# Kernel optimization log

Measured on AMD Instinct MI355X. Metric: run time of the kernel, lower is better.

The kernel has to match this reference:

```python
import jax, jax.numpy as jnp
import numpy as np

B, T, P, I, H, O = 64, 32, 64, 256, 128, 88  # batch, time_steps, pitch_steps, input, hidden, output


def setup_inputs() -> dict:
    key = jax.random.key(0)
    ks = jax.random.split(key, 11)
    s = 0.05
    return {
        "x": jax.random.normal(ks[0], (B, T, P, I), jnp.float32),
        # stacked [fwd, bwd] direction weights, PyTorch LSTM gate order (i, f, g, o)
        "Wt_ih": jax.random.normal(ks[1], (2, 4 * H, I), jnp.float32) * s,
        "Wt_hh": jax.random.normal(ks[2], (2, 4 * H, H), jnp.float32) * s,
        "bt_ih": jax.random.normal(ks[3], (2, 4 * H), jnp.float32) * s,
        "bt_hh": jax.random.normal(ks[4], (2, 4 * H), jnp.float32) * s,
        "Wp_ih": jax.random.normal(ks[5], (2, 4 * H, 2 * H), jnp.float32) * s,
        "Wp_hh": jax.random.normal(ks[6], (2, 4 * H, H), jnp.float32) * s,
        "bp_ih": jax.random.normal(ks[7], (2, 4 * H), jnp.float32) * s,
        "bp_hh": jax.random.normal(ks[8], (2, 4 * H), jnp.float32) * s,
        "Wo": jax.random.normal(ks[9], (O, 2 * H), jnp.float32) * s,
        "bo": jax.random.normal(ks[10], (O,), jnp.float32) * s,
    }


def _cell(xt, h, c, Wih, Whh, bih, bhh):
    # PyTorch LSTMCell math, gate order i, f, g, o
    g = xt @ Wih.T + h @ Whh.T + bih + bhh  # [B, 4H]
    i, f, gc, o = jnp.split(g, 4, axis=-1)
    c2 = jax.nn.sigmoid(f) * c + jax.nn.sigmoid(i) * jnp.tanh(gc)
    h2 = jax.nn.sigmoid(o) * jnp.tanh(c2)
    return h2, c2


def reference(x, Wt_ih, Wt_hh, bt_ih, bt_hh, Wp_ih, Wp_hh, bp_ih, bp_hh, Wo, bo):
    b = x.shape[0]
    xs = x.reshape(b, T * P, I).transpose(1, 0, 2)  # [T*P, B, I] grid flattened in (t, p) order
    z = jnp.zeros((b, H), x.dtype)
    carry0 = (z, z, z, z, z, z, z, z)

    def step(carry, xt):
        htf, ctf, htb, ctb, hpf, cpf, hpb, cpb = carry
        # time LSTM: seq_len==1 so both directions see the same single step, state carried across grid
        htf, ctf = _cell(xt, htf, ctf, Wt_ih[0], Wt_hh[0], bt_ih[0], bt_hh[0])
        htb, ctb = _cell(xt, htb, ctb, Wt_ih[1], Wt_hh[1], bt_ih[1], bt_hh[1])
        tout = jnp.concatenate([htf, htb], axis=-1)  # [B, 2H]
        # pitch LSTM consumes time_out
        hpf, cpf = _cell(tout, hpf, cpf, Wp_ih[0], Wp_hh[0], bp_ih[0], bp_hh[0])
        hpb, cpb = _cell(tout, hpb, cpb, Wp_ih[1], Wp_hh[1], bp_ih[1], bp_hh[1])
        return (htf, ctf, htb, ctb, hpf, cpf, hpb, cpb), None

    carry, _ = jax.lax.scan(step, carry0, xs)
    pitch_out = jnp.concatenate([carry[4], carry[6]], axis=-1)  # last-step pitch output [B, 2H]
    return pitch_out @ Wo.T + bo  # [B, O]
```

## Files before the change

### kernel.cpp

```cpp
#include <hip/hip_runtime.h>
#include <hip/hip_fp16.h>
#include <stdint.h>


typedef _Float16 f16;
typedef _Float16 f16x2 __attribute__((ext_vector_type(2)));
typedef _Float16 f16x4 __attribute__((ext_vector_type(4)));
typedef _Float16 f16x8 __attribute__((ext_vector_type(8)));
typedef float f32x4 __attribute__((ext_vector_type(4)));

#if defined(__has_builtin)
#if __has_builtin(__builtin_amdgcn_fdot2)
#define HAVE_FDOT2 1
#endif
#if __has_builtin(__builtin_amdgcn_rcpf)
#define FRCP(x) __builtin_amdgcn_rcpf(x)
#else
#define FRCP(x) (1.f / (x))
#endif
#if __has_builtin(__builtin_amdgcn_exp2f)
#define FEXP2(x) __builtin_amdgcn_exp2f(x)
#else
#define FEXP2(x) __exp2f(x)
#endif
#endif

static __device__ __forceinline__ float fdot2a(uint32_t a, uint32_t b, float c) {
#ifdef HAVE_FDOT2
    return __builtin_amdgcn_fdot2(__builtin_bit_cast(f16x2, a),
                                  __builtin_bit_cast(f16x2, b), c, false);
#else
    f16x2 av = __builtin_bit_cast(f16x2, a), bv = __builtin_bit_cast(f16x2, b);
    return c + (float)av.x * (float)bv.x + (float)av.y * (float)bv.y;
#endif
}

template <int CTRL>
static __device__ __forceinline__ float qperm(float v) {
    int r = __builtin_amdgcn_update_dpp(0, __builtin_bit_cast(int, v), CTRL, 0xf, 0xf, true);
    return __builtin_bit_cast(float, r);
}


__global__ __launch_bounds__(256) void k_convert_x(const float* __restrict__ x,
                                                   f16* __restrict__ xh) {
    size_t id = (size_t)blockIdx.x * 256 + threadIdx.x;
    const float4* src = (const float4*)(x + id * 8);
    float4 v0 = src[0], v1 = src[1];
    f16x8 o = {(f16)v0.x, (f16)v0.y, (f16)v0.z, (f16)v0.w,
               (f16)v1.x, (f16)v1.y, (f16)v1.z, (f16)v1.w};
    *(f16x8*)(xh + id * 8) = o;
}

__global__ __launch_bounds__(256) void k_convert_w(const float* __restrict__ src,
                                                   f16* __restrict__ dst, int n8) {
    int id = blockIdx.x * 256 + threadIdx.x;
    if (id >= n8) return;
    const float4* sp = (const float4*)(src + (size_t)id * 8);
    float4 v0 = sp[0], v1 = sp[1];
    f16x8 o = {(f16)v0.x, (f16)v0.y, (f16)v0.z, (f16)v0.w,
               (f16)v1.x, (f16)v1.y, (f16)v1.z, (f16)v1.w};
    *(f16x8*)(dst + (size_t)id * 8) = o;
}


#define BM 128
#define BN 128
#define BKK 32
#define LDT 40

__global__ __launch_bounds__(256) void k_gemm(const f16* __restrict__ A,
                                              const f16* __restrict__ B,
                                              f16* __restrict__ C,
                                              const float* __restrict__ bias0,
                                              const float* __restrict__ bias1,
                                              int M, int N, int K) {
    __shared__ __align__(16) f16 As[BM * LDT];
    __shared__ __align__(16) f16 Bs[BN * LDT];
    const int tid  = threadIdx.x;
    const int m0   = blockIdx.x * BM;
    const int n0   = blockIdx.y * BN;
    const int lane = tid & 63;
    const int wave = tid >> 6;
    const int wm   = (wave & 1) * 64;
    const int wn   = (wave >> 1) * 64;
    const int r    = tid >> 1;
    const int koff = (tid & 1) * 16;
    const int mrow = lane & 15;
    const int kof  = (lane >> 4) * 8;

    float bb[4];
#pragma unroll
    for (int j = 0; j < 4; ++j) {
        int cn = n0 + wn + j * 16 + (lane & 15);
        bb[j] = bias0[cn] + bias1[cn];
    }

    f32x4 acc[4][4];
#pragma unroll
    for (int i = 0; i < 4; ++i)
#pragma unroll
        for (int j = 0; j < 4; ++j) acc[i][j] = (f32x4){0.f, 0.f, 0.f, 0.f};

    for (int k0 = 0; k0 < K; k0 += BKK) {
        uint4 a0 = *(const uint4*)(A + (size_t)(m0 + r) * K + k0 + koff);
        uint4 a1 = *(const uint4*)(A + (size_t)(m0 + r) * K + k0 + koff + 8);
        uint4 b0 = *(const uint4*)(B + (size_t)(n0 + r) * K + k0 + koff);
        uint4 b1 = *(const uint4*)(B + (size_t)(n0 + r) * K + k0 + koff + 8);
        *(uint4*)(As + r * LDT + koff)     = a0;
        *(uint4*)(As + r * LDT + koff + 8) = a1;
        *(uint4*)(Bs + r * LDT + koff)     = b0;
        *(uint4*)(Bs + r * LDT + koff + 8) = b1;
        __syncthreads();
        f16x8 af[4], bfr[4];
#pragma unroll
        for (int i = 0; i < 4; ++i)
            af[i] = *(const f16x8*)(As + (wm + i * 16 + mrow) * LDT + kof);
#pragma unroll
        for (int j = 0; j < 4; ++j)
            bfr[j] = *(const f16x8*)(Bs + (wn + j * 16 + mrow) * LDT + kof);
#pragma unroll
        for (int i = 0; i < 4; ++i)
#pragma unroll
            for (int j = 0; j < 4; ++j)
                acc[i][j] = __builtin_amdgcn_mfma_f32_16x16x32_f16(af[i], bfr[j], acc[i][j], 0, 0, 0);
        __syncthreads();
    }
    const int crow = (lane >> 4) * 4;
#pragma unroll
    for (int i = 0; i < 4; ++i) {
#pragma unroll
        for (int j = 0; j < 4; ++j) {
            int cn = n0 + wn + j * 16 + (lane & 15);
            int m  = m0 + wm + i * 16 + crow;
            int bbk = m >> 11;
            int s   = m & 2047;
            f16x4 v = {(f16)(acc[i][j][0] + bb[j]), (f16)(acc[i][j][1] + bb[j]),
                       (f16)(acc[i][j][2] + bb[j]), (f16)(acc[i][j][3] + bb[j])};
            size_t addr = ((((size_t)(s >> 3) * 64 + bbk) * 1024) + cn) * 8 + (s & 7);
            *(f16x4*)(C + addr) = v;
        }
    }
}


__global__ void __attribute__((amdgpu_flat_work_group_size(512, 512),
                               amdgpu_waves_per_eu(2, 2))) k_lstm(
    const f16* __restrict__ G,
    const f16* __restrict__ Whh,
    f16* __restrict__ tout,
    float* __restrict__ hfin,
    const int S, const int flags) {
    const int b   = blockIdx.x >> 1;
    const int dir = blockIdx.x & 1;
    const int t   = threadIdx.x;
    const int u   = t >> 2;
    const int kc  = t & 3;

    __shared__ __align__(16) f16 hb[2][128];

    uint32_t w[4][16];
#pragma unroll
    for (int q = 0; q < 4; ++q) {
        const uint4* wp = (const uint4*)(Whh + ((size_t)(dir * 512 + q * 128 + u) * 128 + kc * 32));
#pragma unroll
        for (int jj = 0; jj < 4; ++jj) {
            uint4 qd = wp[jj];
            w[q][4 * jj + 0] = qd.x; w[q][4 * jj + 1] = qd.y;
            w[q][4 * jj + 2] = qd.z; w[q][4 * jj + 3] = qd.w;
        }
    }
#pragma unroll
    for (int q = 0; q < 4; ++q)
#pragma unroll
        for (int i = 0; i < 16; ++i) __asm__("" : "+v"(w[q][i]));

    const int rowg = dir * 512 + kc * 128 + u;
    const float kact = (kc == 2) ? 2.8853900818f : 1.4426950409f;
    const float Bact = (kc == 2) ? 2.0f : 1.0f;
    const float mk0 = (kc == 0) ? 1.f : 0.f;
    const float mk1 = (kc == 1) ? 1.f : 0.f;
    const float mk2 = (kc == 2) ? 1.f : 0.f;
    const float mk3 = (kc == 3) ? 1.f : 0.f;

    if (t < 64) ((uint32_t*)hb)[64 + t] = 0u;
    float c = 0.f, h = 0.f;
    __syncthreads();

    const f16* gp = G + ((size_t)b * 1024 + rowg) * 8;
    f16* toutp = tout + ((size_t)b * 2048) * 256 + dir * 128 + (t & 15) * 8;

    uint4 gblk = *(const uint4*)(gp);
    for (int sb = 0; sb < S; sb += 8) {
        const size_t nblk = (size_t)((sb + 8 < S) ? (sb >> 3) + 1 : (sb >> 3));
        uint4 gnblk = *(const uint4*)(gp + nblk * 524288);
#pragma unroll
        for (int j = 0; j < 8; ++j) {
            const int s = sb + j;
            f16* hcur = hb[j & 1];
            const f16* hprv = hb[(j & 1) ^ 1];
            if ((flags & 1) && t < 16 && s > 0) {
                uint4 hv16 = *(const uint4*)(hprv + t * 8);
                *(uint4*)(toutp + (size_t)(s - 1) * 256) = hv16;
            }
            float p0a = 0.f, p1a = 0.f, p2a = 0.f, p3a = 0.f;
            float p0b = 0.f, p1b = 0.f, p2b = 0.f, p3b = 0.f;
            const uint4* hv = (const uint4*)(hprv + kc * 32);
#pragma unroll
            for (int jj = 0; jj < 4; ++jj) {
                uint4 hq = hv[jj];
                p0a = fdot2a(w[0][4 * jj + 0], hq.x, p0a);
                p1a = fdot2a(w[1][4 * jj + 0], hq.x, p1a);
                p2a = fdot2a(w[2][4 * jj + 0], hq.x, p2a);
                p3a = fdot2a(w[3][4 * jj + 0], hq.x, p3a);
                p0b = fdot2a(w[0][4 * jj + 1], hq.y, p0b);
                p1b = fdot2a(w[1][4 * jj + 1], hq.y, p1b);
                p2b = fdot2a(w[2][4 * jj + 1], hq.y, p2b);
                p3b = fdot2a(w[3][4 * jj + 1], hq.y, p3b);
                p0a = fdot2a(w[0][4 * jj + 2], hq.z, p0a);
                p1a = fdot2a(w[1][4 * jj + 2], hq.z, p1a);
                p2a = fdot2a(w[2][4 * jj + 2], hq.z, p2a);
                p3a = fdot2a(w[3][4 * jj + 2], hq.z, p3a);
                p0b = fdot2a(w[0][4 * jj + 3], hq.w, p0b);
                p1b = fdot2a(w[1][4 * jj + 3], hq.w, p1b);
                p2b = fdot2a(w[2][4 * jj + 3], hq.w, p2b);
                p3b = fdot2a(w[3][4 * jj + 3], hq.w, p3b);
            }
            float p0 = p0a + p0b, p1 = p1a + p1b, p2 = p2a + p2b, p3 = p3a + p3b;
            {
                uint32_t d = ((const uint32_t*)&gblk)[j >> 1];
                uint16_t us = (uint16_t)((j & 1) ? (d >> 16) : (d & 0xffff));
                float gxb = (float)__builtin_bit_cast(f16, us);
                p0 = __builtin_fmaf(mk0, gxb, p0);
                p1 = __builtin_fmaf(mk1, gxb, p1);
                p2 = __builtin_fmaf(mk2, gxb, p2);
                p3 = __builtin_fmaf(mk3, gxb, p3);
            }
            p0 += qperm<0xB1>(p0); p1 += qperm<0xB1>(p1);
            p2 += qperm<0xB1>(p2); p3 += qperm<0xB1>(p3);
            p0 += qperm<0x4E>(p0); p1 += qperm<0x4E>(p1);
            p2 += qperm<0x4E>(p2); p3 += qperm<0x4E>(p3);
            float v = (kc == 0) ? p0 : (kc == 1) ? p1 : (kc == 2) ? p2 : p3;
            float act = __builtin_fmaf(-Bact, FRCP(1.f + FEXP2(v * kact)), 1.f);
            float gi = qperm<0x00>(act);
            float gf = qperm<0x55>(act);
            float gg = qperm<0xAA>(act);
            float go = qperm<0xFF>(act);
            c = __builtin_fmaf(gf, c, gi * gg);
            float tc = __builtin_fmaf(-2.f, FRCP(1.f + FEXP2(c * 2.8853900818f)), 1.f);
            h = go * tc;
            if (kc == 0) hcur[u] = (f16)h;
            __asm__ __volatile__("s_waitcnt lgkmcnt(0)\n\ts_barrier" ::: "memory");
        }
        gblk = gnblk;
    }
    if ((flags & 1) && t < 16) {
        uint4 hv16 = *(const uint4*)(hb[(2048 - 1) & 1] + t * 8);
        *(uint4*)(toutp + (size_t)(S - 1) * 256) = hv16;
    }
    if ((flags & 2) && kc == 0) hfin[b * 256 + dir * 128 + u] = h;
}


__global__ __launch_bounds__(128) void k_out(const float* __restrict__ hp,
                                             const float* __restrict__ Wo,
                                             const float* __restrict__ bo,
                                             float* __restrict__ out) {
    const int b = blockIdx.x;
    const int t = threadIdx.x;
    __shared__ float hs[256];
    hs[t] = hp[b * 256 + t];
    hs[t + 128] = hp[b * 256 + 128 + t];
    __syncthreads();
    if (t < 88) {
        float acc = bo[t];
        const float* wr = Wo + t * 256;
#pragma unroll 4
        for (int k = 0; k < 256; ++k) acc += wr[k] * hs[k];
        out[b * 88 + t] = acc;
    }
}


extern "C" void kernel_launch(void* const* d_in, const int* in_sizes, int n_in,
                              void* d_out, int out_size, void* d_ws, size_t ws_size,
                              hipStream_t stream) {
    const float* x    = (const float*)d_in[0];
    const float* Wtih = (const float*)d_in[1];
    const float* Wthh = (const float*)d_in[2];
    const float* btih = (const float*)d_in[3];
    const float* bthh = (const float*)d_in[4];
    const float* Wpih = (const float*)d_in[5];
    const float* Wphh = (const float*)d_in[6];
    const float* bpih = (const float*)d_in[7];
    const float* bphh = (const float*)d_in[8];
    const float* Wo   = (const float*)d_in[9];
    const float* bo   = (const float*)d_in[10];

    char* ws = (char*)d_ws;
    f16*   xh    = (f16*)(ws + 0);
    f16*   G     = (f16*)(ws + 67108864);
    f16*   tout  = (f16*)(ws + 335544320);
    f16*   wtih  = (f16*)(ws + 402653184);
    f16*   wthh  = (f16*)(ws + 403177472);
    f16*   wpih  = (f16*)(ws + 403439616);
    f16*   wphh  = (f16*)(ws + 403963904);
    float* hp    = (float*)(ws + 404226048);

    k_convert_x<<<16384, 256, 0, stream>>>(x, xh);
    k_convert_w<<<128, 256, 0, stream>>>(Wtih, wtih, 32768);
    k_convert_w<<<64,  256, 0, stream>>>(Wthh, wthh, 16384);
    k_convert_w<<<128, 256, 0, stream>>>(Wpih, wpih, 32768);
    k_convert_w<<<64,  256, 0, stream>>>(Wphh, wphh, 16384);

    k_gemm<<<dim3(1024, 8), 256, 0, stream>>>(xh, wtih, G, btih, bthh, 131072, 1024, 256);
    k_lstm<<<128, 512, 0, stream>>>(G, wthh, tout, nullptr, 2048, 1);
    k_gemm<<<dim3(1024, 8), 256, 0, stream>>>(tout, wpih, G, bpih, bphh, 131072, 1024, 256);
    k_lstm<<<128, 512, 0, stream>>>(G, wphh, nullptr, hp, 2048, 2);
    k_out<<<64, 128, 0, stream>>>(hp, Wo, bo, (float*)d_out);
}
```

Measured before the change: 2.612 ms.

## Process two batch rows per LSTM workgroup with padded ring buffer and batched output writes

Each LSTM workgroup now runs two batch elements per direction with shared register-resident weights, so the grid halves to 64 blocks and each barrier covers two recurrent steps. Hidden states go into a 16-slot padded LDS ring, which avoids bank conflicts and lets the tout stores be written once every 8 steps by all threads instead of every step by 16 threads. The butterfly reduction is also reworked to use fewer cross-lane permutes. The trade-off is twice the serial work per block and fewer blocks, meaning lower parallelism across CUs.

```diff
diff --git a/kernel.cpp b/kernel.cpp
--- a/kernel.cpp
+++ b/kernel.cpp
@@ -144,6 +144,58 @@
 }
 
 
+
+static __device__ __forceinline__ float lstm_step(
+    f16* __restrict__ rb, int slr, int slw,
+    const uint32_t (&w)[4][16], float gxb, int kc, int u,
+    float kact, float Bact, float& c) {
+    const f16* hpv = rb + slr * 160 + kc * 40;
+    float p0a = 0.f, p1a = 0.f, p2a = 0.f, p3a = 0.f;
+    float p0b = 0.f, p1b = 0.f, p2b = 0.f, p3b = 0.f;
+#pragma unroll
+    for (int jj = 0; jj < 4; ++jj) {
+        uint4 hq = *(const uint4*)(hpv + jj * 8);
+        p0a = fdot2a(w[0][4 * jj + 0], hq.x, p0a);
+        p1a = fdot2a(w[1][4 * jj + 0], hq.x, p1a);
+        p2a = fdot2a(w[2][4 * jj + 0], hq.x, p2a);
+        p3a = fdot2a(w[3][4 * jj + 0], hq.x, p3a);
+        p0b = fdot2a(w[0][4 * jj + 1], hq.y, p0b);
+        p1b = fdot2a(w[1][4 * jj + 1], hq.y, p1b);
+        p2b = fdot2a(w[2][4 * jj + 1], hq.y, p2b);
+        p3b = fdot2a(w[3][4 * jj + 1], hq.y, p3b);
+        p0a = fdot2a(w[0][4 * jj + 2], hq.z, p0a);
+        p1a = fdot2a(w[1][4 * jj + 2], hq.z, p1a);
+        p2a = fdot2a(w[2][4 * jj + 2], hq.z, p2a);
+        p3a = fdot2a(w[3][4 * jj + 2], hq.z, p3a);
+        p0b = fdot2a(w[0][4 * jj + 3], hq.w, p0b);
+        p1b = fdot2a(w[1][4 * jj + 3], hq.w, p1b);
+        p2b = fdot2a(w[2][4 * jj + 3], hq.w, p2b);
+        p3b = fdot2a(w[3][4 * jj + 3], hq.w, p3b);
+    }
+    float p0 = p0a + p0b, p1 = p1a + p1b, p2 = p2a + p2b, p3 = p3a + p3b;
+    const bool k1 = (kc & 1) != 0;
+    const bool k2 = (kc & 2) != 0;
+    float s1 = k1 ? p0 : p1;
+    float s2 = k1 ? p2 : p3;
+    float r1 = qperm<0xB1>(s1);
+    float r2 = qperm<0xB1>(s2);
+    float b1 = (k1 ? p1 : p0) + r1;
+    float b2 = (k1 ? p3 : p2) + r2;
+    float s3 = k2 ? b1 : b2;
+    float r3 = qperm<0x4E>(s3);
+    float v  = (k2 ? b2 : b1) + r3 + gxb;
+    float act = __builtin_fmaf(-Bact, FRCP(1.f + FEXP2(v * kact)), 1.f);
+    float gi = qperm<0x00>(act);
+    float gf = qperm<0x55>(act);
+    float gg = qperm<0xAA>(act);
+    float go = qperm<0xFF>(act);
+    c = __builtin_fmaf(gf, c, gi * gg);
+    float tc = __builtin_fmaf(-2.f, FRCP(1.f + FEXP2(c * 2.8853900818f)), 1.f);
+    float h = go * tc;
+    if (kc == 0) *(rb + slw * 160 + ((u >> 5) * 40 + (u & 31))) = (f16)h;
+    return h;
+}
+
 __global__ void __attribute__((amdgpu_flat_work_group_size(512, 512),
                                amdgpu_waves_per_eu(2, 2))) k_lstm(
     const f16* __restrict__ G,
@@ -151,13 +203,14 @@
     f16* __restrict__ tout,
     float* __restrict__ hfin,
     const int S, const int flags) {
-    const int b   = blockIdx.x >> 1;
-    const int dir = blockIdx.x & 1;
+    const int wg  = blockIdx.x;
+    const int dir = wg >> 5;
+    const int b0  = (wg & 31) * 2;
     const int t   = threadIdx.x;
     const int u   = t >> 2;
     const int kc  = t & 3;
 
-    __shared__ __align__(16) f16 hb[2][128];
+    __shared__ __align__(16) f16 ring[2][16][160];
 
     uint32_t w[4][16];
 #pragma unroll
@@ -178,87 +231,67 @@
     const int rowg = dir * 512 + kc * 128 + u;
     const float kact = (kc == 2) ? 2.8853900818f : 1.4426950409f;
     const float Bact = (kc == 2) ? 2.0f : 1.0f;
-    const float mk0 = (kc == 0) ? 1.f : 0.f;
-    const float mk1 = (kc == 1) ? 1.f : 0.f;
-    const float mk2 = (kc == 2) ? 1.f : 0.f;
-    const float mk3 = (kc == 3) ? 1.f : 0.f;
-
-    if (t < 64) ((uint32_t*)hb)[64 + t] = 0u;
-    float c = 0.f, h = 0.f;
+
+    {
+        uint32_t* rz = (uint32_t*)ring;
+        if (t < 80) { rz[1200 + t] = 0u; rz[2480 + t] = 0u; }
+    }
+    float cA = 0.f, hA = 0.f, cB = 0.f, hB = 0.f;
     __syncthreads();
 
-    const f16* gp = G + ((size_t)b * 1024 + rowg) * 8;
-    f16* toutp = tout + ((size_t)b * 2048) * 256 + dir * 128 + (t & 15) * 8;
-
-    uint4 gblk = *(const uint4*)(gp);
+    const f16* gpA = G + ((size_t)b0 * 1024 + rowg) * 8;
+    const f16* gpB = G + ((size_t)(b0 + 1) * 1024 + rowg) * 8;
+
+    const int fq  = t >> 8;
+    const int frm = t & 255;
+    const int fjf = frm >> 5;
+    const int fc8 = frm & 31;
+
+    uint4 gblkA = *(const uint4*)gpA;
+    uint4 gblkB = *(const uint4*)gpB;
     for (int sb = 0; sb < S; sb += 8) {
         const size_t nblk = (size_t)((sb + 8 < S) ? (sb >> 3) + 1 : (sb >> 3));
-        uint4 gnblk = *(const uint4*)(gp + nblk * 524288);
+        uint4 gnA = *(const uint4*)(gpA + nblk * 524288);
+        uint4 gnB = *(const uint4*)(gpB + nblk * 524288);
+        if ((flags & 1) && sb > 0) {
+            const int sl = ((sb - 8) & 15) + fjf;
+            const f16* rp = &ring[fq][sl][(fc8 >> 3) * 40 + (fc8 & 7) * 4];
+            uint2 hv = *(const uint2*)rp;
+            f16* op = tout + ((size_t)(b0 + fq) * 2048 + (sb - 8 + fjf)) * 256 + dir * 128 + fc8 * 4;
+            *(uint2*)op = hv;
+        }
 #pragma unroll
         for (int j = 0; j < 8; ++j) {
-            const int s = sb + j;
-            f16* hcur = hb[j & 1];
-            const f16* hprv = hb[(j & 1) ^ 1];
-            if ((flags & 1) && t < 16 && s > 0) {
-                uint4 hv16 = *(const uint4*)(hprv + t * 8);
-                *(uint4*)(toutp + (size_t)(s - 1) * 256) = hv16;
-            }
-            float p0a = 0.f, p1a = 0.f, p2a = 0.f, p3a = 0.f;
-            float p0b = 0.f, p1b = 0.f, p2b = 0.f, p3b = 0.f;
-            const uint4* hv = (const uint4*)(hprv + kc * 32);
-#pragma unroll
-            for (int jj = 0; jj < 4; ++jj) {
-                uint4 hq = hv[jj];
-                p0a = fdot2a(w[0][4 * jj + 0], hq.x, p0a);
-                p1a = fdot2a(w[1][4 * jj + 0], hq.x, p1a);
-                p2a = fdot2a(w[2][4 * jj + 0], hq.x, p2a);
-                p3a = fdot2a(w[3][4 * jj + 0], hq.x, p3a);
-                p0b = fdot2a(w[0][4 * jj + 1], hq.y, p0b);
-                p1b = fdot2a(w[1][4 * jj + 1], hq.y, p1b);
-                p2b = fdot2a(w[2][4 * jj + 1], hq.y, p2b);
-                p3b = fdot2a(w[3][4 * jj + 1], hq.y, p3b);
-                p0a = fdot2a(w[0][4 * jj + 2], hq.z, p0a);
-                p1a = fdot2a(w[1][4 * jj + 2], hq.z, p1a);
-                p2a = fdot2a(w[2][4 * jj + 2], hq.z, p2a);
-                p3a = fdot2a(w[3][4 * jj + 2], hq.z, p3a);
-                p0b = fdot2a(w[0][4 * jj + 3], hq.w, p0b);
-                p1b = fdot2a(w[1][4 * jj + 3], hq.w, p1b);
-                p2b = fdot2a(w[2][4 * jj + 3], hq.w, p2b);
-                p3b = fdot2a(w[3][4 * jj + 3], hq.w, p3b);
-            }
-            float p0 = p0a + p0b, p1 = p1a + p1b, p2 = p2a + p2b, p3 = p3a + p3b;
+            const int slr = (sb + j + 15) & 15;
+            const int slw = (sb + j) & 15;
             {
-                uint32_t d = ((const uint32_t*)&gblk)[j >> 1];
+                uint32_t d = ((const uint32_t*)&gblkA)[j >> 1];
                 uint16_t us = (uint16_t)((j & 1) ? (d >> 16) : (d & 0xffff));
                 float gxb = (float)__builtin_bit_cast(f16, us);
-                p0 = __builtin_fmaf(mk0, gxb, p0);
-                p1 = __builtin_fmaf(mk1, gxb, p1);
-                p2 = __builtin_fmaf(mk2, gxb, p2);
-                p3 = __builtin_fmaf(mk3, gxb, p3);
+                hA = lstm_step(&ring[0][0][0], slr, slw, w, gxb, kc, u, kact, Bact, cA);
             }
-            p0 += qperm<0xB1>(p0); p1 += qperm<0xB1>(p1);
-            p2 += qperm<0xB1>(p2); p3 += qperm<0xB1>(p3);
-            p0 += qperm<0x4E>(p0); p1 += qperm<0x4E>(p1);
-            p2 += qperm<0x4E>(p2); p3 += qperm<0x4E>(p3);
-            float v = (kc == 0) ? p0 : (kc == 1) ? p1 : (kc == 2) ? p2 : p3;
-            float act = __builtin_fmaf(-Bact, FRCP(1.f + FEXP2(v * kact)), 1.f);
-            float gi = qperm<0x00>(act);
-            float gf = qperm<0x55>(act);
-            float gg = qperm<0xAA>(act);
-            float go = qperm<0xFF>(act);
-            c = __builtin_fmaf(gf, c, gi * gg);
-            float tc = __builtin_fmaf(-2.f, FRCP(1.f + FEXP2(c * 2.8853900818f)), 1.f);
-            h = go * tc;
-            if (kc == 0) hcur[u] = (f16)h;
+            {
+                uint32_t d = ((const uint32_t*)&gblkB)[j >> 1];
+                uint16_t us = (uint16_t)((j & 1) ? (d >> 16) : (d & 0xffff));
+                float gxb = (float)__builtin_bit_cast(f16, us);
+                hB = lstm_step(&ring[1][0][0], slr, slw, w, gxb, kc, u, kact, Bact, cB);
+            }
             __asm__ __volatile__("s_waitcnt lgkmcnt(0)\n\ts_barrier" ::: "memory");
         }
-        gblk = gnblk;
-    }
-    if ((flags & 1) && t < 16) {
-        uint4 hv16 = *(const uint4*)(hb[(2048 - 1) & 1] + t * 8);
-        *(uint4*)(toutp + (size_t)(S - 1) * 256) = hv16;
-    }
-    if ((flags & 2) && kc == 0) hfin[b * 256 + dir * 128 + u] = h;
+        gblkA = gnA;
+        gblkB = gnB;
+    }
+    if (flags & 1) {
+        const int sl = ((S - 8) & 15) + fjf;
+        const f16* rp = &ring[fq][sl][(fc8 >> 3) * 40 + (fc8 & 7) * 4];
+        uint2 hv = *(const uint2*)rp;
+        f16* op = tout + ((size_t)(b0 + fq) * 2048 + (S - 8 + fjf)) * 256 + dir * 128 + fc8 * 4;
+        *(uint2*)op = hv;
+    }
+    if ((flags & 2) && kc == 0) {
+        hfin[(b0 + 0) * 256 + dir * 128 + u] = hA;
+        hfin[(b0 + 1) * 256 + dir * 128 + u] = hB;
+    }
 }
 
 
@@ -314,8 +347,8 @@
     k_convert_w<<<64,  256, 0, stream>>>(Wphh, wphh, 16384);
 
     k_gemm<<<dim3(1024, 8), 256, 0, stream>>>(xh, wtih, G, btih, bthh, 131072, 1024, 256);
-    k_lstm<<<128, 512, 0, stream>>>(G, wthh, tout, nullptr, 2048, 1);
+    k_lstm<<<64, 512, 0, stream>>>(G, wthh, tout, nullptr, 2048, 1);
     k_gemm<<<dim3(1024, 8), 256, 0, stream>>>(tout, wpih, G, bpih, bphh, 131072, 1024, 256);
-    k_lstm<<<128, 512, 0, stream>>>(G, wphh, nullptr, hp, 2048, 2);
+    k_lstm<<<64, 512, 0, stream>>>(G, wphh, nullptr, hp, 2048, 2);
     k_out<<<64, 128, 0, stream>>>(hp, Wo, bo, (float*)d_out);
 }
```

Result: slower. 4.365 ms (+67.1%).

## Use MFMA for LSTM recurrence with 16 batches per block and gate-interleaved weights

Applied to the files above, without the earlier changes.

Moves the recurrent h@Whh product from per-thread fdot2 with DPP reductions to MFMA 16x16x32. Each block now handles 16 batch rows for one direction, so the launch drops from 128 blocks to 8. Weights and biases are pre-permuted so the four gates of each unit sit together, with the sigmoid/tanh log2e scale folded in, and the GEMM is transposed so its output lands in the layout the new LSTM reads. This cuts per-step instruction count and reduction shuffles, but leaves only 8 blocks on the GPU for the serial recurrence, so occupancy is very low.

```diff
diff --git a/kernel.cpp b/kernel.cpp
--- a/kernel.cpp
+++ b/kernel.cpp
@@ -4,15 +4,11 @@
 
 
 typedef _Float16 f16;
-typedef _Float16 f16x2 __attribute__((ext_vector_type(2)));
 typedef _Float16 f16x4 __attribute__((ext_vector_type(4)));
 typedef _Float16 f16x8 __attribute__((ext_vector_type(8)));
 typedef float f32x4 __attribute__((ext_vector_type(4)));
 
 #if defined(__has_builtin)
-#if __has_builtin(__builtin_amdgcn_fdot2)
-#define HAVE_FDOT2 1
-#endif
 #if __has_builtin(__builtin_amdgcn_rcpf)
 #define FRCP(x) __builtin_amdgcn_rcpf(x)
 #else
@@ -25,20 +21,12 @@
 #endif
 #endif
 
-static __device__ __forceinline__ float fdot2a(uint32_t a, uint32_t b, float c) {
-#ifdef HAVE_FDOT2
-    return __builtin_amdgcn_fdot2(__builtin_bit_cast(f16x2, a),
-                                  __builtin_bit_cast(f16x2, b), c, false);
-#else
-    f16x2 av = __builtin_bit_cast(f16x2, a), bv = __builtin_bit_cast(f16x2, b);
-    return c + (float)av.x * (float)bv.x + (float)av.y * (float)bv.y;
-#endif
-}
-
-template <int CTRL>
-static __device__ __forceinline__ float qperm(float v) {
-    int r = __builtin_amdgcn_update_dpp(0, __builtin_bit_cast(int, v), CTRL, 0xf, 0xf, true);
-    return __builtin_bit_cast(float, r);
+#define K_SIG 1.4426950409f
+#define K_TANH 2.8853900818f
+
+static __device__ __forceinline__ f16x8 mk8(uint32_t x, uint32_t y, uint32_t z, uint32_t w) {
+    uint4 u; u.x = x; u.y = y; u.z = z; u.w = w;
+    return __builtin_bit_cast(f16x8, u);
 }
 
 
@@ -52,15 +40,30 @@
     *(f16x8*)(xh + id * 8) = o;
 }
 
-__global__ __launch_bounds__(256) void k_convert_w(const float* __restrict__ src,
-                                                   f16* __restrict__ dst, int n8) {
+__global__ __launch_bounds__(256) void k_convert_wp(const float* __restrict__ src,
+                                                    f16* __restrict__ dst, int ksh, int n8) {
     int id = blockIdx.x * 256 + threadIdx.x;
     if (id >= n8) return;
-    const float4* sp = (const float4*)(src + (size_t)id * 8);
+    int rp = id >> ksh;
+    int kb = id & ((1 << ksh) - 1);
+    int dd = rp >> 9, gi = rp & 3, q = (rp >> 2) & 127;
+    float sc = (gi == 2) ? K_TANH : K_SIG;
+    size_t so = ((size_t)(dd * 512 + gi * 128 + q) << (ksh + 3)) + kb * 8;
+    const float4* sp = (const float4*)(src + so);
     float4 v0 = sp[0], v1 = sp[1];
-    f16x8 o = {(f16)v0.x, (f16)v0.y, (f16)v0.z, (f16)v0.w,
-               (f16)v1.x, (f16)v1.y, (f16)v1.z, (f16)v1.w};
+    f16x8 o = {(f16)(v0.x * sc), (f16)(v0.y * sc), (f16)(v0.z * sc), (f16)(v0.w * sc),
+               (f16)(v1.x * sc), (f16)(v1.y * sc), (f16)(v1.z * sc), (f16)(v1.w * sc)};
     *(f16x8*)(dst + (size_t)id * 8) = o;
+}
+
+__global__ __launch_bounds__(256) void k_bias(const float* __restrict__ a,
+                                              const float* __restrict__ b,
+                                              float* __restrict__ o) {
+    int rp = blockIdx.x * 256 + threadIdx.x;
+    int dd = rp >> 9, gi = rp & 3, q = (rp >> 2) & 127;
+    int orig = dd * 512 + gi * 128 + q;
+    float sc = (gi == 2) ? K_TANH : K_SIG;
+    o[rp] = (a[orig] + b[orig]) * sc;
 }
 
 
@@ -72,8 +75,7 @@
 __global__ __launch_bounds__(256) void k_gemm(const f16* __restrict__ A,
                                               const f16* __restrict__ B,
                                               f16* __restrict__ C,
-                                              const float* __restrict__ bias0,
-                                              const float* __restrict__ bias1,
+                                              const float* __restrict__ bsum,
                                               int M, int N, int K) {
     __shared__ __align__(16) f16 As[BM * LDT];
     __shared__ __align__(16) f16 Bs[BN * LDT];
@@ -88,13 +90,7 @@
     const int koff = (tid & 1) * 16;
     const int mrow = lane & 15;
     const int kof  = (lane >> 4) * 8;
-
-    float bb[4];
-#pragma unroll
-    for (int j = 0; j < 4; ++j) {
-        int cn = n0 + wn + j * 16 + (lane & 15);
-        bb[j] = bias0[cn] + bias1[cn];
-    }
+    const int crow = (lane >> 4) * 4;
 
     f32x4 acc[4][4];
 #pragma unroll
@@ -126,139 +122,187 @@
                 acc[i][j] = __builtin_amdgcn_mfma_f32_16x16x32_f16(af[i], bfr[j], acc[i][j], 0, 0, 0);
         __syncthreads();
     }
-    const int crow = (lane >> 4) * 4;
 #pragma unroll
     for (int i = 0; i < 4; ++i) {
+        const int rb = m0 + wm + i * 16 + crow;
+        const float4 bbv = *(const float4*)(bsum + rb);
+        const int dd  = rb >> 9;
+        const int rho = rb & 511;
+        const int tb  = rho >> 4;
+        const int wvv = tb >> 2;
+        const int tau = tb & 3;
+        const int hii = (rho >> 2) & 3;
 #pragma unroll
         for (int j = 0; j < 4; ++j) {
-            int cn = n0 + wn + j * 16 + (lane & 15);
-            int m  = m0 + wm + i * 16 + crow;
-            int bbk = m >> 11;
-            int s   = m & 2047;
-            f16x4 v = {(f16)(acc[i][j][0] + bb[j]), (f16)(acc[i][j][1] + bb[j]),
-                       (f16)(acc[i][j][2] + bb[j]), (f16)(acc[i][j][3] + bb[j])};
-            size_t addr = ((((size_t)(s >> 3) * 64 + bbk) * 1024) + cn) * 8 + (s & 7);
-            *(f16x4*)(C + addr) = v;
+            const int cm = n0 + wn + j * 16 + (lane & 15);
+            const int b  = cm >> 11;
+            const int s  = cm & 2047;
+            const int gw = dd * 4 + (b >> 4);
+            const int ch = b & 15;
+            const int ln = hii * 16 + ch;
+            size_t addr = (size_t)s * 131072 +
+                          (size_t)(gw * 16384 + wvv * 2048 + ln * 32 + tau * 8);
+            f16x4 v = {(f16)(acc[i][j][0] + bbv.x), (f16)(acc[i][j][1] + bbv.y),
+                       (f16)(acc[i][j][2] + bbv.z), (f16)(acc[i][j][3] + bbv.w)};
+            *(f16x4*)((char*)C + addr) = v;
         }
     }
 }
 
 
-__global__ void __attribute__((amdgpu_flat_work_group_size(512, 512),
-                               amdgpu_waves_per_eu(2, 2))) k_lstm(
+template <int MODE>
+__global__ void __attribute__((amdgpu_flat_work_group_size(512, 512))) k_lstm(
     const f16* __restrict__ G,
     const f16* __restrict__ Whh,
     f16* __restrict__ tout,
     float* __restrict__ hfin,
-    const int S, const int flags) {
-    const int b   = blockIdx.x >> 1;
-    const int dir = blockIdx.x & 1;
-    const int t   = threadIdx.x;
-    const int u   = t >> 2;
-    const int kc  = t & 3;
-
-    __shared__ __align__(16) f16 hb[2][128];
+    const int S) {
+    const int g  = blockIdx.x;
+    const int d  = g >> 2, bb = g & 3;
+    const int t  = threadIdx.x;
+    const int l  = t & 63, wv = t >> 6;
+    const int hi = l >> 4, ch = l & 15;
+
+    __shared__ __align__(16) char hx[16384];
 
     uint32_t w[4][16];
 #pragma unroll
-    for (int q = 0; q < 4; ++q) {
-        const uint4* wp = (const uint4*)(Whh + ((size_t)(dir * 512 + q * 128 + u) * 128 + kc * 32));
-#pragma unroll
-        for (int jj = 0; jj < 4; ++jj) {
-            uint4 qd = wp[jj];
-            w[q][4 * jj + 0] = qd.x; w[q][4 * jj + 1] = qd.y;
-            w[q][4 * jj + 2] = qd.z; w[q][4 * jj + 3] = qd.w;
+    for (int tau = 0; tau < 4; ++tau) {
+        const f16* wr = Whh + (size_t)(d * 512 + (4 * wv + tau) * 16 + ch) * 128 + hi * 8;
+#pragma unroll
+        for (int ks = 0; ks < 4; ++ks) {
+            uint4 q = *(const uint4*)(wr + ks * 32);
+            w[tau][ks * 4 + 0] = q.x; w[tau][ks * 4 + 1] = q.y;
+            w[tau][ks * 4 + 2] = q.z; w[tau][ks * 4 + 3] = q.w;
         }
     }
 #pragma unroll
-    for (int q = 0; q < 4; ++q)
-#pragma unroll
-        for (int i = 0; i < 16; ++i) __asm__("" : "+v"(w[q][i]));
-
-    const int rowg = dir * 512 + kc * 128 + u;
-    const float kact = (kc == 2) ? 2.8853900818f : 1.4426950409f;
-    const float Bact = (kc == 2) ? 2.0f : 1.0f;
-    const float mk0 = (kc == 0) ? 1.f : 0.f;
-    const float mk1 = (kc == 1) ? 1.f : 0.f;
-    const float mk2 = (kc == 2) ? 1.f : 0.f;
-    const float mk3 = (kc == 3) ? 1.f : 0.f;
-
-    if (t < 64) ((uint32_t*)hb)[64 + t] = 0u;
-    float c = 0.f, h = 0.f;
+    for (int tau = 0; tau < 4; ++tau)
+#pragma unroll
+        for (int i = 0; i < 16; ++i) __asm__("" : "+v"(w[tau][i]));
+
+    for (int i = t; i < 4096; i += 512) ((uint32_t*)hx)[i] = 0;
+
+    const int lds_rd = ch * 272 + hi * 16;
+    const int lds_wr = ch * 272 + 32 * wv + 2 * hi;
+    const int lds_f  = (t >> 5) * 272 + (t & 31) * 8;
+
+    f16* tbase = nullptr;
+    if (MODE == 1)
+        tbase = tout + ((size_t)(bb * 16 + (t >> 5)) * 2048) * 256 + d * 128 + (t & 31) * 4;
+
+    const char* gp = (const char*)G + (size_t)(g * 16384 + wv * 2048 + l * 32);
+    uint4 qa[4], qb[4];
+#pragma unroll
+    for (int j = 0; j < 4; ++j) {
+        qa[j] = *(const uint4*)(gp + (size_t)j * 131072);
+        qb[j] = *(const uint4*)(gp + (size_t)j * 131072 + 16);
+    }
+
+    float c0 = 0.f, c1 = 0.f, c2 = 0.f, c3 = 0.f;
+    int pofs = 0;
     __syncthreads();
 
-    const f16* gp = G + ((size_t)b * 1024 + rowg) * 8;
-    f16* toutp = tout + ((size_t)b * 2048) * 256 + dir * 128 + (t & 15) * 8;
-
-    uint4 gblk = *(const uint4*)(gp);
-    for (int sb = 0; sb < S; sb += 8) {
-        const size_t nblk = (size_t)((sb + 8 < S) ? (sb >> 3) + 1 : (sb >> 3));
-        uint4 gnblk = *(const uint4*)(gp + nblk * 524288);
-#pragma unroll
-        for (int j = 0; j < 8; ++j) {
+    for (int sb = 0; sb < S; sb += 4) {
+#pragma unroll
+        for (int j = 0; j < 4; ++j) {
             const int s = sb + j;
-            f16* hcur = hb[j & 1];
-            const f16* hprv = hb[(j & 1) ^ 1];
-            if ((flags & 1) && t < 16 && s > 0) {
-                uint4 hv16 = *(const uint4*)(hprv + t * 8);
-                *(uint4*)(toutp + (size_t)(s - 1) * 256) = hv16;
-            }
-            float p0a = 0.f, p1a = 0.f, p2a = 0.f, p3a = 0.f;
-            float p0b = 0.f, p1b = 0.f, p2b = 0.f, p3b = 0.f;
-            const uint4* hv = (const uint4*)(hprv + kc * 32);
-#pragma unroll
-            for (int jj = 0; jj < 4; ++jj) {
-                uint4 hq = hv[jj];
-                p0a = fdot2a(w[0][4 * jj + 0], hq.x, p0a);
-                p1a = fdot2a(w[1][4 * jj + 0], hq.x, p1a);
-                p2a = fdot2a(w[2][4 * jj + 0], hq.x, p2a);
-                p3a = fdot2a(w[3][4 * jj + 0], hq.x, p3a);
-                p0b = fdot2a(w[0][4 * jj + 1], hq.y, p0b);
-                p1b = fdot2a(w[1][4 * jj + 1], hq.y, p1b);
-                p2b = fdot2a(w[2][4 * jj + 1], hq.y, p2b);
-                p3b = fdot2a(w[3][4 * jj + 1], hq.y, p3b);
-                p0a = fdot2a(w[0][4 * jj + 2], hq.z, p0a);
-                p1a = fdot2a(w[1][4 * jj + 2], hq.z, p1a);
-                p2a = fdot2a(w[2][4 * jj + 2], hq.z, p2a);
-                p3a = fdot2a(w[3][4 * jj + 2], hq.z, p3a);
-                p0b = fdot2a(w[0][4 * jj + 3], hq.w, p0b);
-                p1b = fdot2a(w[1][4 * jj + 3], hq.w, p1b);
-                p2b = fdot2a(w[2][4 * jj + 3], hq.w, p2b);
-                p3b = fdot2a(w[3][4 * jj + 3], hq.w, p3b);
-            }
-            float p0 = p0a + p0b, p1 = p1a + p1b, p2 = p2a + p2b, p3 = p3a + p3b;
-            {
-                uint32_t d = ((const uint32_t*)&gblk)[j >> 1];
-                uint16_t us = (uint16_t)((j & 1) ? (d >> 16) : (d & 0xffff));
-                float gxb = (float)__builtin_bit_cast(f16, us);
-                p0 = __builtin_fmaf(mk0, gxb, p0);
-                p1 = __builtin_fmaf(mk1, gxb, p1);
-                p2 = __builtin_fmaf(mk2, gxb, p2);
-                p3 = __builtin_fmaf(mk3, gxb, p3);
-            }
-            p0 += qperm<0xB1>(p0); p1 += qperm<0xB1>(p1);
-            p2 += qperm<0xB1>(p2); p3 += qperm<0xB1>(p3);
-            p0 += qperm<0x4E>(p0); p1 += qperm<0x4E>(p1);
-            p2 += qperm<0x4E>(p2); p3 += qperm<0x4E>(p3);
-            float v = (kc == 0) ? p0 : (kc == 1) ? p1 : (kc == 2) ? p2 : p3;
-            float act = __builtin_fmaf(-Bact, FRCP(1.f + FEXP2(v * kact)), 1.f);
-            float gi = qperm<0x00>(act);
-            float gf = qperm<0x55>(act);
-            float gg = qperm<0xAA>(act);
-            float go = qperm<0xFF>(act);
-            c = __builtin_fmaf(gf, c, gi * gg);
-            float tc = __builtin_fmaf(-2.f, FRCP(1.f + FEXP2(c * 2.8853900818f)), 1.f);
-            h = go * tc;
-            if (kc == 0) hcur[u] = (f16)h;
+            if (MODE == 1 && s > 0) {
+                const char* fp = hx + (pofs + lds_f);
+                uint2 hv;
+                hv.x = *(const uint32_t*)fp;
+                hv.y = *(const uint32_t*)(fp + 4);
+                *(uint2*)(tbase + (size_t)(s - 1) * 256) = hv;
+            }
+            const char* hb = hx + (pofs + lds_rd);
+            f16x8 b0 = *(const f16x8*)(hb);
+            f16x8 b1 = *(const f16x8*)(hb + 64);
+            f16x8 b2 = *(const f16x8*)(hb + 128);
+            f16x8 b3 = *(const f16x8*)(hb + 192);
+            f16x8 ga = __builtin_bit_cast(f16x8, qa[j]);
+            f16x8 gb = __builtin_bit_cast(f16x8, qb[j]);
+            f32x4 A0 = {(float)ga[0], (float)ga[1], (float)ga[2], (float)ga[3]};
+            f32x4 A1 = {(float)ga[4], (float)ga[5], (float)ga[6], (float)ga[7]};
+            f32x4 A2 = {(float)gb[0], (float)gb[1], (float)gb[2], (float)gb[3]};
+            f32x4 A3 = {(float)gb[4], (float)gb[5], (float)gb[6], (float)gb[7]};
+            {
+                int sn = s + 4; if (sn > S - 1) sn = S - 1;
+                qa[j] = *(const uint4*)(gp + (size_t)sn * 131072);
+                qb[j] = *(const uint4*)(gp + (size_t)sn * 131072 + 16);
+            }
+            A0 = __builtin_amdgcn_mfma_f32_16x16x32_f16(mk8(w[0][0], w[0][1], w[0][2], w[0][3]), b0, A0, 0, 0, 0);
+            A1 = __builtin_amdgcn_mfma_f32_16x16x32_f16(mk8(w[1][0], w[1][1], w[1][2], w[1][3]), b0, A1, 0, 0, 0);
+            A2 = __builtin_amdgcn_mfma_f32_16x16x32_f16(mk8(w[2][0], w[2][1], w[2][2], w[2][3]), b0, A2, 0, 0, 0);
+            A3 = __builtin_amdgcn_mfma_f32_16x16x32_f16(mk8(w[3][0], w[3][1], w[3][2], w[3][3]), b0, A3, 0, 0, 0);
+            A0 = __builtin_amdgcn_mfma_f32_16x16x32_f16(mk8(w[0][4], w[0][5], w[0][6], w[0][7]), b1, A0, 0, 0, 0);
+            A1 = __builtin_amdgcn_mfma_f32_16x16x32_f16(mk8(w[1][4], w[1][5], w[1][6], w[1][7]), b1, A1, 0, 0, 0);
+            A2 = __builtin_amdgcn_mfma_f32_16x16x32_f16(mk8(w[2][4], w[2][5], w[2][6], w[2][7]), b1, A2, 0, 0, 0);
+            A3 = __builtin_amdgcn_mfma_f32_16x16x32_f16(mk8(w[3][4], w[3][5], w[3][6], w[3][7]), b1, A3, 0, 0, 0);
+            A0 = __builtin_amdgcn_mfma_f32_16x16x32_f16(mk8(w[0][8], w[0][9], w[0][10], w[0][11]), b2, A0, 0, 0, 0);
+            A1 = __builtin_amdgcn_mfma_f32_16x16x32_f16(mk8(w[1][8], w[1][9], w[1][10], w[1][11]), b2, A1, 0, 0, 0);
+            A2 = __builtin_amdgcn_mfma_f32_16x16x32_f16(mk8(w[2][8], w[2][9], w[2][10], w[2][11]), b2, A2, 0, 0, 0);
+            A3 = __builtin_amdgcn_mfma_f32_16x16x32_f16(mk8(w[3][8], w[3][9], w[3][10], w[3][11]), b2, A3, 0, 0, 0);
+            A0 = __builtin_amdgcn_mfma_f32_16x16x32_f16(mk8(w[0][12], w[0][13], w[0][14], w[0][15]), b3, A0, 0, 0, 0);
+            A1 = __builtin_amdgcn_mfma_f32_16x16x32_f16(mk8(w[1][12], w[1][13], w[1][14], w[1][15]), b3, A1, 0, 0, 0);
+            A2 = __builtin_amdgcn_mfma_f32_16x16x32_f16(mk8(w[2][12], w[2][13], w[2][14], w[2][15]), b3, A2, 0, 0, 0);
+            A3 = __builtin_amdgcn_mfma_f32_16x16x32_f16(mk8(w[3][12], w[3][13], w[3][14], w[3][15]), b3, A3, 0, 0, 0);
+            float h0, h1, h2, h3;
+            {
+                float si = FRCP(1.f + FEXP2(-A0[0]));
+                float sf = FRCP(1.f + FEXP2(-A0[1]));
+                float tg = __builtin_fmaf(-2.f, FRCP(1.f + FEXP2(A0[2])), 1.f);
+                float so = FRCP(1.f + FEXP2(-A0[3]));
+                c0 = __builtin_fmaf(sf, c0, si * tg);
+                float tc = __builtin_fmaf(-2.f, FRCP(1.f + FEXP2(c0 * K_TANH)), 1.f);
+                h0 = so * tc;
+            }
+            {
+                float si = FRCP(1.f + FEXP2(-A1[0]));
+                float sf = FRCP(1.f + FEXP2(-A1[1]));
+                float tg = __builtin_fmaf(-2.f, FRCP(1.f + FEXP2(A1[2])), 1.f);
+                float so = FRCP(1.f + FEXP2(-A1[3]));
+                c1 = __builtin_fmaf(sf, c1, si * tg);
+                float tc = __builtin_fmaf(-2.f, FRCP(1.f + FEXP2(c1 * K_TANH)), 1.f);
+                h1 = so * tc;
+            }
+            {
+                float si = FRCP(1.f + FEXP2(-A2[0]));
+                float sf = FRCP(1.f + FEXP2(-A2[1]));
+                float tg = __builtin_fmaf(-2.f, FRCP(1.f + FEXP2(A2[2])), 1.f);
+                float so = FRCP(1.f + FEXP2(-A2[3]));
+                c2 = __builtin_fmaf(sf, c2, si * tg);
+                float tc = __builtin_fmaf(-2.f, FRCP(1.f + FEXP2(c2 * K_TANH)), 1.f);
+                h2 = so * tc;
+            }
+            {
+                float si = FRCP(1.f + FEXP2(-A3[0]));
+                float sf = FRCP(1.f + FEXP2(-A3[1]));
+                float tg = __builtin_fmaf(-2.f, FRCP(1.f + FEXP2(A3[2])), 1.f);
+                float so = FRCP(1.f + FEXP2(-A3[3]));
+                c3 = __builtin_fmaf(sf, c3, si * tg);
+                float tc = __builtin_fmaf(-2.f, FRCP(1.f + FEXP2(c3 * K_TANH)), 1.f);
+                h3 = so * tc;
+            }
+            if (MODE == 2 && s == S - 1) {
+                float* hf = hfin + (size_t)(bb * 16 + ch) * 256 + d * 128 + 16 * wv + hi;
+                hf[0] = h0; hf[4] = h1; hf[8] = h2; hf[12] = h3;
+            }
+            char* hw = hx + ((pofs ^ 8192) + lds_wr);
+            *(f16*)(hw)      = (f16)h0;
+            *(f16*)(hw + 8)  = (f16)h1;
+            *(f16*)(hw + 16) = (f16)h2;
+            *(f16*)(hw + 24) = (f16)h3;
             __asm__ __volatile__("s_waitcnt lgkmcnt(0)\n\ts_barrier" ::: "memory");
+            pofs ^= 8192;
         }
-        gblk = gnblk;
-    }
-    if ((flags & 1) && t < 16) {
-        uint4 hv16 = *(const uint4*)(hb[(2048 - 1) & 1] + t * 8);
-        *(uint4*)(toutp + (size_t)(S - 1) * 256) = hv16;
-    }
-    if ((flags & 2) && kc == 0) hfin[b * 256 + dir * 128 + u] = h;
+    }
+    if (MODE == 1) {
+        const char* fp = hx + lds_f;
+        uint2 hv;
+        hv.x = *(const uint32_t*)fp;
+        hv.y = *(const uint32_t*)(fp + 4);
+        *(uint2*)(tbase + (size_t)(S - 1) * 256) = hv;
+    }
 }
 
 
@@ -305,17 +349,21 @@
     f16*   wthh  = (f16*)(ws + 403177472);
     f16*   wpih  = (f16*)(ws + 403439616);
     f16*   wphh  = (f16*)(ws + 403963904);
+    float* bsT   = (float*)(ws + 404226048);
+    float* bsP   = (float*)(ws + 404230144);
     float* hp    = (float*)(ws + 404226048);
 
     k_convert_x<<<16384, 256, 0, stream>>>(x, xh);
-    k_convert_w<<<128, 256, 0, stream>>>(Wtih, wtih, 32768);
-    k_convert_w<<<64,  256, 0, stream>>>(Wthh, wthh, 16384);
-    k_convert_w<<<128, 256, 0, stream>>>(Wpih, wpih, 32768);
-    k_convert_w<<<64,  256, 0, stream>>>(Wphh, wphh, 16384);
-
-    k_gemm<<<dim3(1024, 8), 256, 0, stream>>>(xh, wtih, G, btih, bthh, 131072, 1024, 256);
-    k_lstm<<<128, 512, 0, stream>>>(G, wthh, tout, nullptr, 2048, 1);
-    k_gemm<<<dim3(1024, 8), 256, 0, stream>>>(tout, wpih, G, bpih, bphh, 131072, 1024, 256);
-    k_lstm<<<128, 512, 0, stream>>>(G, wphh, nullptr, hp, 2048, 2);
+    k_convert_wp<<<128, 256, 0, stream>>>(Wtih, wtih, 5, 32768);
+    k_convert_wp<<<64,  256, 0, stream>>>(Wthh, wthh, 4, 16384);
+    k_convert_wp<<<128, 256, 0, stream>>>(Wpih, wpih, 5, 32768);
+    k_convert_wp<<<64,  256, 0, stream>>>(Wphh, wphh, 4, 16384);
+    k_bias<<<4, 256, 0, stream>>>(btih, bthh, bsT);
+    k_bias<<<4, 256, 0, stream>>>(bpih, bphh, bsP);
+
+    k_gemm<<<dim3(8, 1024), 256, 0, stream>>>(wtih, xh, G, bsT, 1024, 131072, 256);
+    k_lstm<1><<<8, 512, 0, stream>>>(G, wthh, tout, nullptr, 2048);
+    k_gemm<<<dim3(8, 1024), 256, 0, stream>>>(wpih, tout, G, bsP, 1024, 131072, 256);
+    k_lstm<2><<<8, 512, 0, stream>>>(G, wphh, nullptr, hp, 2048);
     k_out<<<64, 128, 0, stream>>>(hp, Wo, bo, (float*)d_out);
 }
```

Result: slower. 4.030 ms (+54.3%).
